# Kernel tuning notes

Hardware: AMD Instinct MI355X
Metric: run time of the kernel (lower is better)

## Reference

```python
import jax, jax.numpy as jnp
import numpy as np

DIM = 1024
KV_DIM = 768
NUM_HEADS = 16
HEAD_DIM = DIM // NUM_HEADS
EPS = 1e-6


def _rms_norm(h, g):
    var = jnp.mean(h * h, axis=-1, keepdims=True)
    return h * jax.lax.rsqrt(var + EPS) * g


def _rotate_half(t):
    t1, t2 = jnp.split(t, 2, axis=-1)
    return jnp.concatenate((-t2, t1), axis=-1)


def _apply_rope(t, cos, sin):
    # t: [B, L, H, D]; cos/sin: [B, L, D] -> broadcast over heads (unsqueeze_dim=2)
    cos = cos[:, :, None, :]
    sin = sin[:, :, None, :]
    return t * cos + _rotate_half(t) * sin


def setup_inputs() -> dict:
    key = jax.random.key(0)
    ks = jax.random.split(key, 16)
    B, Lq, Lkv = 2, 4096, 1024
    inp = {
        "x": jax.random.normal(ks[0], (B, Lq, DIM), jnp.float32),
        "y": jax.random.normal(ks[1], (B, Lkv, KV_DIM), jnp.float32),
        "x_cos": jax.random.normal(ks[2], (B, Lq, HEAD_DIM), jnp.float32),
        "x_sin": jax.random.normal(ks[3], (B, Lq, HEAD_DIM), jnp.float32),
        "y_cos": jax.random.normal(ks[4], (B, Lkv, HEAD_DIM), jnp.float32),
        "y_sin": jax.random.normal(ks[5], (B, Lkv, HEAD_DIM), jnp.float32),
        # Linear params stored as [in, out] (apply as h @ W + b)
        "Wq": jax.random.normal(ks[6], (DIM, DIM), jnp.float32) * 0.02,
        "bq": jnp.zeros((DIM,), jnp.float32),
        "Wk": jax.random.normal(ks[7], (KV_DIM, DIM), jnp.float32) * 0.02,
        "bk": jnp.zeros((DIM,), jnp.float32),
        "Wv": jax.random.normal(ks[8], (KV_DIM, DIM), jnp.float32) * 0.02,
        "bv": jnp.zeros((DIM,), jnp.float32),
        "Wo": jax.random.normal(ks[9], (DIM, DIM), jnp.float32) * 0.02,
        "bo": jnp.zeros((DIM,), jnp.float32),
        "gq": jnp.ones((DIM,), jnp.float32),   # RMSNorm weight for q
        "gk": jnp.ones((DIM,), jnp.float32),   # RMSNorm weight for k
    }
    return inp


def reference(x, y, x_cos, x_sin, y_cos, y_sin,
              Wq, bq, Wk, bk, Wv, bv, Wo, bo, gq, gk):
    B, Lq, _ = x.shape
    _, Lkv, _ = y.shape
    q = _rms_norm(x @ Wq + bq, gq)              # [B, Lq, DIM]
    k = _rms_norm(y @ Wk + bk, gk)              # [B, Lkv, DIM]
    v = y @ Wv + bv                              # [B, Lkv, DIM]

    q = q.reshape(B, Lq, NUM_HEADS, HEAD_DIM)
    k = k.reshape(B, Lkv, NUM_HEADS, HEAD_DIM)
    v = v.reshape(B, Lkv, NUM_HEADS, HEAD_DIM)

    q = _apply_rope(q, x_cos, x_sin)
    k = _apply_rope(k, y_cos, y_sin)

    scale = HEAD_DIM ** -0.5
    scores = jnp.einsum("blhd,bmhd->bhlm", q, k) * scale   # [B, H, Lq, Lkv]
    probs = jax.nn.softmax(scores, axis=-1)
    out = jnp.einsum("bhlm,bmhd->blhd", probs, v)           # [B, Lq, H, D]
    out = out.reshape(B, Lq, DIM)
    return out @ Wo + bo
```

## Files before the change

### kernel.cpp

```cpp
#include <hip/hip_runtime.h>

typedef __bf16 bf16;
typedef __bf16 bf16x4 __attribute__((ext_vector_type(4)));
typedef __bf16 bf16x8 __attribute__((ext_vector_type(8)));
typedef float  f32x4  __attribute__((ext_vector_type(4)));

#define NH   16
#define HD   64
#define DQ   1024
#define DKV  768
#define LQ   4096
#define LKV  1024
#define NB   2

__device__ __forceinline__ f32x4 mfma16(bf16x8 a, bf16x8 b, f32x4 c) {
    return __builtin_amdgcn_mfma_f32_16x16x32_bf16(a, b, c, 0, 0, 0);
}

#define GLDS16(g, l) __builtin_amdgcn_global_load_lds(                      \
    (const __attribute__((address_space(1))) void*)(g),                     \
    (__attribute__((address_space(3))) void*)(l), 16, 0, 0)

__global__ __launch_bounds__(256) void prep(
        const float* __restrict__ Wq, const float* __restrict__ Wk,
        const float* __restrict__ Wv, const float* __restrict__ Wo,
        bf16* __restrict__ Wq_t, bf16* __restrict__ Wk_t,
        bf16* __restrict__ Wv_t, bf16* __restrict__ Wo_t,
        const float* __restrict__ x, const float* __restrict__ y,
        bf16* __restrict__ xb, bf16* __restrict__ yb,
        int nx8, int ntot8) {
    if (blockIdx.z < 4) {
        __shared__ float tile[32][33];
        const float* in; bf16* out; int K;
        switch (blockIdx.z) {
            case 0:  in = Wq; out = Wq_t; K = DQ;  break;
            case 1:  in = Wk; out = Wk_t; K = DKV; break;
            case 2:  in = Wv; out = Wv_t; K = DKV; break;
            default: in = Wo; out = Wo_t; K = DQ;  break;
        }
        int n0 = blockIdx.x * 32, k0 = blockIdx.y * 32;
        if (k0 >= K) return;
        int tx = threadIdx.x, ty = threadIdx.y;
        for (int yy = 0; yy < 32; yy += 8)
            tile[ty + yy][tx] = in[(size_t)(k0 + ty + yy) * DQ + n0 + tx];
        __syncthreads();
        for (int yy = 0; yy < 32; yy += 8)
            out[(size_t)(n0 + ty + yy) * K + k0 + tx] = (bf16)tile[tx][ty + yy];
    } else {
        int tid = threadIdx.y * 32 + threadIdx.x;
        int flat = (blockIdx.y * 32 + blockIdx.x) * 256 + tid;
        for (int i = flat; i < ntot8; i += 32 * 32 * 256) {
            const float* in; bf16* out; int j;
            if (i < nx8) { in = x; out = xb; j = i; }
            else         { in = y; out = yb; j = i - nx8; }
            float4 a0 = ((const float4*)in)[(size_t)j * 2];
            float4 a1 = ((const float4*)in)[(size_t)j * 2 + 1];
            bf16x8 v = {(bf16)a0.x, (bf16)a0.y, (bf16)a0.z, (bf16)a0.w,
                        (bf16)a1.x, (bf16)a1.y, (bf16)a1.z, (bf16)a1.w};
            ((bf16x8*)out)[j] = v;
        }
    }
}

template <int MODE>
__device__ __forceinline__ void gemm_body(const bf16* __restrict__ A,
                                          const bf16* __restrict__ Bt,
                                          const float* __restrict__ bias,
                                          void* __restrict__ Cv,
                                          int N, int K, int m0) {
    __shared__ bf16 As[128 * 32];
    __shared__ bf16 Bs[128 * 32];
    int tid  = threadIdx.x;
    int lane = tid & 63, w = tid >> 6;
    int quad = lane >> 4, l15 = lane & 15;
    int wm = (w >> 1) * 64, wn = (w & 1) * 64;
    int n0 = blockIdx.x * 128;
    int srow = tid >> 2, scol = (tid & 3) * 8;
    const bf16* Ag = &A [(size_t)(m0 + srow) * K + scol];
    const bf16* Bg = &Bt[(size_t)(n0 + srow) * K + scol];
    bf16* Asw = As + w * 512;
    bf16* Bsw = Bs + w * 512;

    f32x4 acc[4][4] = {};

    for (int k0 = 0; k0 < K; k0 += 32) {
        GLDS16(Ag + k0,                  Asw);
        GLDS16(Ag + (size_t)64 * K + k0, Asw + 2048);
        GLDS16(Bg + k0,                  Bsw);
        GLDS16(Bg + (size_t)64 * K + k0, Bsw + 2048);
        __syncthreads();
        bf16x8 af[4], bfr[4];
#pragma unroll
        for (int i = 0; i < 4; i++)
            af[i] = *(const bf16x8*)&As[(size_t)(wm + i * 16 + l15) * 32 + quad * 8];
#pragma unroll
        for (int j = 0; j < 4; j++)
            bfr[j] = *(const bf16x8*)&Bs[(size_t)(wn + j * 16 + l15) * 32 + quad * 8];
#pragma unroll
        for (int i = 0; i < 4; i++)
#pragma unroll
            for (int j = 0; j < 4; j++)
                acc[i][j] = mfma16(af[i], bfr[j], acc[i][j]);
        __syncthreads();
    }

    bf16*  Cb = (bf16*)Cv;
    float* Cf = (float*)Cv;
#pragma unroll
    for (int i = 0; i < 4; i++)
#pragma unroll
        for (int j = 0; j < 4; j++) {
            int col = n0 + wn + j * 16 + l15;
            float bcol = bias[col];
            if (MODE == 1) {
                int rowb = m0 + wm + i * 16 + quad * 4;
                int bb = rowb >> 10, kv = rowb & 1023;
                int h = col >> 6, d = col & 63;
                bf16x4 val = {(bf16)(acc[i][j][0] + bcol), (bf16)(acc[i][j][1] + bcol),
                              (bf16)(acc[i][j][2] + bcol), (bf16)(acc[i][j][3] + bcol)};
                *(bf16x4*)&Cb[(((size_t)(bb * NH + h) * HD) + d) * LKV + kv] = val;
            } else {
#pragma unroll
                for (int r = 0; r < 4; r++) {
                    int row = m0 + wm + i * 16 + quad * 4 + r;
                    float v = acc[i][j][r] + bcol;
                    if (MODE == 2) Cf[(size_t)row * N + col] = v;
                    else           Cb[(size_t)row * N + col] = (bf16)v;
                }
            }
        }
}

__global__ __launch_bounds__(256) void gemm_qkv(
        const bf16* xb, const bf16* Wq_t, const float* bq, bf16* qbuf,
        const bf16* yb, const bf16* Wk_t, const float* bk, bf16* kbuf,
        const bf16* Wv_t, const float* bv, bf16* vT) {
    int y = blockIdx.y;
    if (y < 64)      gemm_body<0>(xb, Wq_t, bq, qbuf, DQ, DQ,  y * 128);
    else if (y < 80) gemm_body<0>(yb, Wk_t, bk, kbuf, DQ, DKV, (y - 64) * 128);
    else             gemm_body<1>(yb, Wv_t, bv, vT,   DQ, DKV, (y - 80) * 128);
}
__global__ __launch_bounds__(256) void gemm_o(const bf16* A, const bf16* Bt,
                                              const float* bias, void* Cv) {
    gemm_body<2>(A, Bt, bias, Cv, DQ, DQ, blockIdx.y * 128);
}

__global__ __launch_bounds__(256) void rmsnorm_rope3(bf16* __restrict__ qb,
                                                     bf16* __restrict__ kb,
                                                     const float* __restrict__ gq,
                                                     const float* __restrict__ gk,
                                                     const float* __restrict__ xc,
                                                     const float* __restrict__ xs,
                                                     const float* __restrict__ yc,
                                                     const float* __restrict__ ys) {
    int w = threadIdx.x >> 6, lane = threadIdx.x & 63;
    int row = blockIdx.x * 4 + w;
    bf16* t; const float *g, *cs, *sn;
    if (row < NB * LQ) {
        t = qb + (size_t)row * DQ; g = gq;
        cs = xc + (size_t)row * HD; sn = xs + (size_t)row * HD;
    } else {
        int r2 = row - NB * LQ;
        t = kb + (size_t)r2 * DQ; g = gk;
        cs = yc + (size_t)r2 * HD; sn = ys + (size_t)r2 * HD;
    }
    int c0 = lane * 16;
    bf16x8 a0 = *(const bf16x8*)&t[c0];
    bf16x8 a1 = *(const bf16x8*)&t[c0 + 8];
    float vv[16], ss = 0.f;
#pragma unroll
    for (int j = 0; j < 8; j++) { vv[j] = (float)a0[j]; vv[8 + j] = (float)a1[j]; }
#pragma unroll
    for (int j = 0; j < 16; j++) ss += vv[j] * vv[j];
#pragma unroll
    for (int off = 32; off >= 1; off >>= 1) ss += __shfl_xor(ss, off, 64);
    float rms = rsqrtf(ss * (1.0f / 1024.0f) + 1e-6f);
    float nv[16];
#pragma unroll
    for (int j = 0; j < 16; j++) nv[j] = vv[j] * rms * g[c0 + j];
    int d0 = (lane & 3) * 16;
    float sgn = (lane & 2) ? 1.f : -1.f;
    bf16x8 o0, o1;
#pragma unroll
    for (int j = 0; j < 16; j++) {
        float pv = __shfl_xor(nv[j], 2, 64);
        float r = nv[j] * cs[d0 + j] + sgn * pv * sn[d0 + j];
        if (j < 8) o0[j] = (bf16)r; else o1[j - 8] = (bf16)r;
    }
    *(bf16x8*)&t[c0]     = o0;
    *(bf16x8*)&t[c0 + 8] = o1;
}

__global__ __launch_bounds__(256) void attn_kern(const bf16* __restrict__ q,
                                                 const bf16* __restrict__ k,
                                                 const bf16* __restrict__ vT,
                                                 bf16* __restrict__ o) {
    __shared__ bf16 Ks[2][64][72];
    __shared__ bf16 Vs[2][64][72];
    __shared__ bf16 pbuf[4][2][16][72];
    int tid = threadIdx.x, w = tid >> 6, lane = tid & 63;
    int quad = lane >> 4, l15 = lane & 15;
    int b = blockIdx.z, h = blockIdx.y, qt = blockIdx.x;
    int qrow0 = qt * 128 + w * 16;

    bf16x8 qf[2][2];
#pragma unroll
    for (int tl = 0; tl < 2; tl++) {
        size_t qb = ((size_t)(b * LQ) + qrow0 + tl * 64 + l15) * DQ + h * HD;
        qf[tl][0] = *(const bf16x8*)&q[qb + quad * 8];
        qf[tl][1] = *(const bf16x8*)&q[qb + 32 + quad * 8];
#pragma unroll
        for (int e = 0; e < 8; e++) {
            qf[tl][0][e] = (bf16)((float)qf[tl][0][e] * 0.125f);
            qf[tl][1][e] = (bf16)((float)qf[tl][1][e] * 0.125f);
        }
    }

    int srow = tid >> 2, scol = (tid & 3) * 16;
    const bf16* kg = &k[((size_t)(b * LKV) + srow) * DQ + h * HD + scol];
    const bf16* vg = &vT[(((size_t)(b * NH + h) * HD) + srow) * LKV + scol];

    bf16x8 kr0 = *(const bf16x8*)kg;
    bf16x8 kr1 = *(const bf16x8*)(kg + 8);
    bf16x8 vr0 = *(const bf16x8*)vg;
    bf16x8 vr1 = *(const bf16x8*)(vg + 8);
    *(bf16x8*)&Ks[0][srow][scol]     = kr0;
    *(bf16x8*)&Ks[0][srow][scol + 8] = kr1;
    *(bf16x8*)&Vs[0][srow][scol]     = vr0;
    *(bf16x8*)&Vs[0][srow][scol + 8] = vr1;
    __syncthreads();

    f32x4 O[2][4] = {};
    float m_run[2] = {-1e30f, -1e30f}, l_run[2] = {0.f, 0.f};

    for (int i = 0; i < 16; i++) {
        int cur = i & 1;
        if (i < 15) {
            size_t ko = (size_t)(i + 1) * 64 * DQ;
            kr0 = *(const bf16x8*)(kg + ko);
            kr1 = *(const bf16x8*)(kg + ko + 8);
            vr0 = *(const bf16x8*)(vg + (i + 1) * 64);
            vr1 = *(const bf16x8*)(vg + (i + 1) * 64 + 8);
        }
        f32x4 S[2][4];
#pragma unroll
        for (int t = 0; t < 4; t++) {
            bf16x8 kf0 = *(const bf16x8*)&Ks[cur][t * 16 + l15][quad * 8];
            bf16x8 kf1 = *(const bf16x8*)&Ks[cur][t * 16 + l15][32 + quad * 8];
#pragma unroll
            for (int tl = 0; tl < 2; tl++) {
                f32x4 z = {};
                z = mfma16(kf0, qf[tl][0], z);
                S[tl][t] = mfma16(kf1, qf[tl][1], z);
            }
        }
#pragma unroll
        for (int tl = 0; tl < 2; tl++) {
            float mx = -1e30f;
#pragma unroll
            for (int t = 0; t < 4; t++)
#pragma unroll
                for (int r = 0; r < 4; r++) mx = fmaxf(mx, S[tl][t][r]);
            mx = fmaxf(mx, __shfl_xor(mx, 16, 64));
            mx = fmaxf(mx, __shfl_xor(mx, 32, 64));
            float mn = fmaxf(m_run[tl], mx);
            float alpha = __expf(m_run[tl] - mn);
            m_run[tl] = mn;
            float rs = 0.f;
#pragma unroll
            for (int t = 0; t < 4; t++) {
                float p0 = __expf(S[tl][t][0] - mn), p1 = __expf(S[tl][t][1] - mn);
                float p2 = __expf(S[tl][t][2] - mn), p3 = __expf(S[tl][t][3] - mn);
                rs += (p0 + p1) + (p2 + p3);
                bf16x4 pb4 = {(bf16)p0, (bf16)p1, (bf16)p2, (bf16)p3};
                *(bf16x4*)&pbuf[w][tl][l15][t * 16 + quad * 4] = pb4;
            }
            rs += __shfl_xor(rs, 16, 64);
            rs += __shfl_xor(rs, 32, 64);
            l_run[tl] = l_run[tl] * alpha + rs;
#pragma unroll
            for (int td = 0; td < 4; td++)
#pragma unroll
                for (int r = 0; r < 4; r++) O[tl][td][r] *= alpha;
        }
        asm volatile("s_waitcnt lgkmcnt(0)" ::: "memory");
#pragma unroll
        for (int tl = 0; tl < 2; tl++) {
            bf16x8 pf0 = *(const bf16x8*)&pbuf[w][tl][l15][quad * 8];
            bf16x8 pf1 = *(const bf16x8*)&pbuf[w][tl][l15][32 + quad * 8];
#pragma unroll
            for (int td = 0; td < 4; td++) {
                bf16x8 vf0 = *(const bf16x8*)&Vs[cur][td * 16 + l15][quad * 8];
                bf16x8 vf1 = *(const bf16x8*)&Vs[cur][td * 16 + l15][32 + quad * 8];
                O[tl][td] = mfma16(vf0, pf0, O[tl][td]);
                O[tl][td] = mfma16(vf1, pf1, O[tl][td]);
            }
        }
        if (i < 15) {
            int nxt = 1 - cur;
            *(bf16x8*)&Ks[nxt][srow][scol]     = kr0;
            *(bf16x8*)&Ks[nxt][srow][scol + 8] = kr1;
            *(bf16x8*)&Vs[nxt][srow][scol]     = vr0;
            *(bf16x8*)&Vs[nxt][srow][scol + 8] = vr1;
            __syncthreads();
        }
    }

#pragma unroll
    for (int tl = 0; tl < 2; tl++) {
        float inv = 1.0f / l_run[tl];
        size_t orow = ((size_t)(b * LQ) + qrow0 + tl * 64 + l15) * DQ + h * HD;
#pragma unroll
        for (int td = 0; td < 4; td++) {
            bf16x4 ov = {(bf16)(O[tl][td][0] * inv), (bf16)(O[tl][td][1] * inv),
                         (bf16)(O[tl][td][2] * inv), (bf16)(O[tl][td][3] * inv)};
            *(bf16x4*)&o[orow + td * 16 + quad * 4] = ov;
        }
    }
}

extern "C" void kernel_launch(void* const* d_in, const int* in_sizes, int n_in,
                              void* d_out, int out_size, void* d_ws, size_t ws_size,
                              hipStream_t stream) {
    const float* x     = (const float*)d_in[0];
    const float* y     = (const float*)d_in[1];
    const float* x_cos = (const float*)d_in[2];
    const float* x_sin = (const float*)d_in[3];
    const float* y_cos = (const float*)d_in[4];
    const float* y_sin = (const float*)d_in[5];
    const float* Wq    = (const float*)d_in[6];
    const float* bq    = (const float*)d_in[7];
    const float* Wk    = (const float*)d_in[8];
    const float* bk    = (const float*)d_in[9];
    const float* Wv    = (const float*)d_in[10];
    const float* bv    = (const float*)d_in[11];
    const float* Wo    = (const float*)d_in[12];
    const float* bo    = (const float*)d_in[13];
    const float* gq    = (const float*)d_in[14];
    const float* gk    = (const float*)d_in[15];

    char* ws = (char*)d_ws;
    bf16* Wq_t = (bf16*)ws;  ws += (size_t)DQ * DQ * 2;
    bf16* Wk_t = (bf16*)ws;  ws += (size_t)DQ * DKV * 2;
    bf16* Wv_t = (bf16*)ws;  ws += (size_t)DQ * DKV * 2;
    bf16* Wo_t = (bf16*)ws;  ws += (size_t)DQ * DQ * 2;
    bf16* qbuf = (bf16*)ws;  ws += (size_t)NB * LQ * DQ * 2;
    bf16* kbuf = (bf16*)ws;  ws += (size_t)NB * LKV * DQ * 2;
    bf16* vT   = (bf16*)ws;  ws += (size_t)NB * NH * HD * LKV * 2;
    bf16* aout = (bf16*)ws;  ws += (size_t)NB * LQ * DQ * 2;
    bf16* yb   = (bf16*)ws;  ws += (size_t)NB * LKV * DKV * 2;
    bf16* xb   = aout;

    int nx8 = NB * LQ * DQ / 8, ny8 = NB * LKV * DKV / 8;
    prep<<<dim3(32, 32, 5), dim3(32, 8), 0, stream>>>(
        Wq, Wk, Wv, Wo, Wq_t, Wk_t, Wv_t, Wo_t,
        x, y, xb, yb, nx8, nx8 + ny8);

    gemm_qkv<<<dim3(8, 96), 256, 0, stream>>>(
        xb, Wq_t, bq, qbuf, yb, Wk_t, bk, kbuf, Wv_t, bv, vT);

    rmsnorm_rope3<<<NB * (LQ + LKV) / 4, 256, 0, stream>>>(
        qbuf, kbuf, gq, gk, x_cos, x_sin, y_cos, y_sin);

    attn_kern<<<dim3(LQ / 128, NH, NB), 256, 0, stream>>>(qbuf, kbuf, vT, aout);

    gemm_o<<<dim3(DQ / 128, NB * LQ / 128), 256, 0, stream>>>(aout, Wo_t, bo, d_out);
}
```

Before: 299.3 us.

## Rewrite attention kernel with 32x32 MFMA, register-resident P, async LDS loads

The attention kernel switches from 16x16x32 to 32x32x16 bf16 MFMA, with each wave owning 32 query rows. The probability tile stays in registers: it is converted with packed bf16 conversion and rearranged with permlane32 swaps instead of a round trip through an LDS buffer. K and V tiles are loaded with global_load_lds into XOR-swizzled, unpadded shared memory, and softmax rescaling is skipped unless the running max grows by more than a threshold. Other changes include raising MFMA priority with s_setprio and requesting 4 blocks per CU through launch bounds. The aim is to cut LDS traffic and instruction overhead in the attention loop, at the cost of heavier register use and correctness that depends on the swizzle and lane-permute layout.

```diff
diff --git a/kernel.cpp b/kernel.cpp
--- a/kernel.cpp
+++ b/kernel.cpp
@@ -4,6 +4,8 @@
 typedef __bf16 bf16x4 __attribute__((ext_vector_type(4)));
 typedef __bf16 bf16x8 __attribute__((ext_vector_type(8)));
 typedef float  f32x4  __attribute__((ext_vector_type(4)));
+typedef float  f32x16 __attribute__((ext_vector_type(16)));
+typedef unsigned u32x4 __attribute__((ext_vector_type(4)));
 
 #define NH   16
 #define HD   64
@@ -15,6 +17,18 @@
 
 __device__ __forceinline__ f32x4 mfma16(bf16x8 a, bf16x8 b, f32x4 c) {
     return __builtin_amdgcn_mfma_f32_16x16x32_bf16(a, b, c, 0, 0, 0);
+}
+__device__ __forceinline__ f32x16 mfma32(bf16x8 a, bf16x8 b, f32x16 c) {
+    return __builtin_amdgcn_mfma_f32_32x32x16_bf16(a, b, c, 0, 0, 0);
+}
+
+__device__ __forceinline__ void plswap(unsigned &a, unsigned &b) {
+#if __has_builtin(__builtin_amdgcn_permlane32_swap)
+    auto r = __builtin_amdgcn_permlane32_swap(a, b, false, false);
+    a = (unsigned)r[0]; b = (unsigned)r[1];
+#else
+    asm volatile("v_permlane32_swap_b32 %0, %1" : "+v"(a), "+v"(b));
+#endif
 }
 
 #define GLDS16(g, l) __builtin_amdgcn_global_load_lds(                      \
@@ -191,130 +205,128 @@
     *(bf16x8*)&t[c0 + 8] = o1;
 }
 
-__global__ __launch_bounds__(256) void attn_kern(const bf16* __restrict__ q,
-                                                 const bf16* __restrict__ k,
-                                                 const bf16* __restrict__ vT,
-                                                 bf16* __restrict__ o) {
-    __shared__ bf16 Ks[2][64][72];
-    __shared__ bf16 Vs[2][64][72];
-    __shared__ bf16 pbuf[4][2][16][72];
+__global__ __launch_bounds__(256, 4) void attn_kern(const bf16* __restrict__ q,
+                                                    const bf16* __restrict__ k,
+                                                    const bf16* __restrict__ vT,
+                                                    bf16* __restrict__ o) {
+    __shared__ bf16 Ks[2][64][64];
+    __shared__ bf16 Vs[2][64][64];
     int tid = threadIdx.x, w = tid >> 6, lane = tid & 63;
-    int quad = lane >> 4, l15 = lane & 15;
+    int l31 = lane & 31, hi = lane >> 5;
     int b = blockIdx.z, h = blockIdx.y, qt = blockIdx.x;
-    int qrow0 = qt * 128 + w * 16;
-
-    bf16x8 qf[2][2];
-#pragma unroll
-    for (int tl = 0; tl < 2; tl++) {
-        size_t qb = ((size_t)(b * LQ) + qrow0 + tl * 64 + l15) * DQ + h * HD;
-        qf[tl][0] = *(const bf16x8*)&q[qb + quad * 8];
-        qf[tl][1] = *(const bf16x8*)&q[qb + 32 + quad * 8];
-#pragma unroll
-        for (int e = 0; e < 8; e++) {
-            qf[tl][0][e] = (bf16)((float)qf[tl][0][e] * 0.125f);
-            qf[tl][1][e] = (bf16)((float)qf[tl][1][e] * 0.125f);
-        }
-    }
-
-    int srow = tid >> 2, scol = (tid & 3) * 16;
-    const bf16* kg = &k[((size_t)(b * LKV) + srow) * DQ + h * HD + scol];
-    const bf16* vg = &vT[(((size_t)(b * NH + h) * HD) + srow) * LKV + scol];
-
-    bf16x8 kr0 = *(const bf16x8*)kg;
-    bf16x8 kr1 = *(const bf16x8*)(kg + 8);
-    bf16x8 vr0 = *(const bf16x8*)vg;
-    bf16x8 vr1 = *(const bf16x8*)(vg + 8);
-    *(bf16x8*)&Ks[0][srow][scol]     = kr0;
-    *(bf16x8*)&Ks[0][srow][scol + 8] = kr1;
-    *(bf16x8*)&Vs[0][srow][scol]     = vr0;
-    *(bf16x8*)&Vs[0][srow][scol + 8] = vr1;
+    int qrow = qt * 128 + w * 32 + l31;
+    int sw8 = (l31 & 7) << 3;
+
+    bf16x8 qf[4];
+    {
+        const bf16* qg = &q[((size_t)(b * LQ) + qrow) * DQ + h * HD + hi * 8];
+#pragma unroll
+        for (int kc = 0; kc < 4; kc++) {
+            bf16x8 tq = *(const bf16x8*)(qg + kc * 16);
+#pragma unroll
+            for (int e = 0; e < 8; e++) tq[e] = (bf16)((float)tq[e] * 0.125f);
+            qf[kc] = tq;
+        }
+    }
+
+    int rb = w * 16;
+    int srow = rb + (lane >> 3);
+    int sl = (lane & 7) ^ (srow & 7);
+    const bf16* kg0 = &k[((size_t)(b * LKV) + srow) * DQ + h * HD + sl * 8];
+    const bf16* vg0 = &vT[(((size_t)(b * NH + h) * HD) + srow) * LKV + sl * 8];
+
+    GLDS16(kg0,                   &Ks[0][rb][0]);
+    GLDS16(kg0 + (size_t)8 * DQ,  &Ks[0][rb + 8][0]);
+    GLDS16(vg0,                   &Vs[0][rb][0]);
+    GLDS16(vg0 + (size_t)8 * LKV, &Vs[0][rb + 8][0]);
     __syncthreads();
 
-    f32x4 O[2][4] = {};
-    float m_run[2] = {-1e30f, -1e30f}, l_run[2] = {0.f, 0.f};
+    f32x16 O0 = {}, O1 = {};
+    float m_run = -1e30f, l_run = 0.f;
 
     for (int i = 0; i < 16; i++) {
         int cur = i & 1;
         if (i < 15) {
+            int nxt = cur ^ 1;
             size_t ko = (size_t)(i + 1) * 64 * DQ;
-            kr0 = *(const bf16x8*)(kg + ko);
-            kr1 = *(const bf16x8*)(kg + ko + 8);
-            vr0 = *(const bf16x8*)(vg + (i + 1) * 64);
-            vr1 = *(const bf16x8*)(vg + (i + 1) * 64 + 8);
-        }
-        f32x4 S[2][4];
-#pragma unroll
-        for (int t = 0; t < 4; t++) {
-            bf16x8 kf0 = *(const bf16x8*)&Ks[cur][t * 16 + l15][quad * 8];
-            bf16x8 kf1 = *(const bf16x8*)&Ks[cur][t * 16 + l15][32 + quad * 8];
-#pragma unroll
-            for (int tl = 0; tl < 2; tl++) {
-                f32x4 z = {};
-                z = mfma16(kf0, qf[tl][0], z);
-                S[tl][t] = mfma16(kf1, qf[tl][1], z);
+            int    vo = (i + 1) * 64;
+            GLDS16(kg0 + ko,                   &Ks[nxt][rb][0]);
+            GLDS16(kg0 + ko + (size_t)8 * DQ,  &Ks[nxt][rb + 8][0]);
+            GLDS16(vg0 + vo,                   &Vs[nxt][rb][0]);
+            GLDS16(vg0 + vo + (size_t)8 * LKV, &Vs[nxt][rb + 8][0]);
+        }
+#pragma unroll
+        for (int t = 0; t < 2; t++) {
+            f32x16 S = {};
+            {
+                int krow = t * 32 + l31;
+                __builtin_amdgcn_s_setprio(1);
+#pragma unroll
+                for (int kc = 0; kc < 4; kc++) {
+                    bf16x8 kf = *(const bf16x8*)&Ks[cur][krow][(kc * 16 + hi * 8) ^ sw8];
+                    S = mfma32(kf, qf[kc], S);
+                }
+                __builtin_amdgcn_s_setprio(0);
             }
-        }
-#pragma unroll
-        for (int tl = 0; tl < 2; tl++) {
-            float mx = -1e30f;
-#pragma unroll
-            for (int t = 0; t < 4; t++)
-#pragma unroll
-                for (int r = 0; r < 4; r++) mx = fmaxf(mx, S[tl][t][r]);
-            mx = fmaxf(mx, __shfl_xor(mx, 16, 64));
-            mx = fmaxf(mx, __shfl_xor(mx, 32, 64));
-            float mn = fmaxf(m_run[tl], mx);
-            float alpha = __expf(m_run[tl] - mn);
-            m_run[tl] = mn;
+            float m01 = fmaxf(fmaxf(S[0], S[1]),  fmaxf(S[2], S[3]));
+            float m23 = fmaxf(fmaxf(S[4], S[5]),  fmaxf(S[6], S[7]));
+            float m45 = fmaxf(fmaxf(S[8], S[9]),  fmaxf(S[10], S[11]));
+            float m67 = fmaxf(fmaxf(S[12], S[13]), fmaxf(S[14], S[15]));
+            float pmax = fmaxf(fmaxf(m01, m23), fmaxf(m45, m67));
+            pmax = fmaxf(pmax, __shfl_xor(pmax, 32, 64));
+            if (!__all(pmax - m_run <= 8.f)) {
+                float mn = fmaxf(m_run, pmax);
+                float alpha = __expf(m_run - mn);
+                m_run = mn; l_run *= alpha;
+#pragma unroll
+                for (int r = 0; r < 16; r++) { O0[r] *= alpha; O1[r] *= alpha; }
+            }
             float rs = 0.f;
 #pragma unroll
-            for (int t = 0; t < 4; t++) {
-                float p0 = __expf(S[tl][t][0] - mn), p1 = __expf(S[tl][t][1] - mn);
-                float p2 = __expf(S[tl][t][2] - mn), p3 = __expf(S[tl][t][3] - mn);
-                rs += (p0 + p1) + (p2 + p3);
-                bf16x4 pb4 = {(bf16)p0, (bf16)p1, (bf16)p2, (bf16)p3};
-                *(bf16x4*)&pbuf[w][tl][l15][t * 16 + quad * 4] = pb4;
+            for (int r = 0; r < 16; r++) { S[r] = __expf(S[r] - m_run); rs += S[r]; }
+            rs += __shfl_xor(rs, 32, 64);
+            l_run += rs;
+            unsigned dw[8];
+#pragma unroll
+            for (int g = 0; g < 4; g++)
+#pragma unroll
+                for (int hh = 0; hh < 2; hh++) {
+                    unsigned d_;
+                    asm("v_cvt_pk_bf16_f32 %0, %1, %2"
+                        : "=v"(d_) : "v"(S[4 * g + 2 * hh]), "v"(S[4 * g + 2 * hh + 1]));
+                    dw[g * 2 + hh] = d_;
+                }
+#pragma unroll
+            for (int kcl = 0; kcl < 2; kcl++) {
+                int kc = t * 2 + kcl;
+                unsigned a0 = dw[(2 * kcl) * 2 + 0], b0 = dw[(2 * kcl + 1) * 2 + 0];
+                unsigned a1 = dw[(2 * kcl) * 2 + 1], b1 = dw[(2 * kcl + 1) * 2 + 1];
+                plswap(a0, b0);
+                plswap(a1, b1);
+                u32x4 pw = {a0, a1, b0, b1};
+                bf16x8 pb = __builtin_bit_cast(bf16x8, pw);
+                int vcol = (kc * 16 + hi * 8) ^ sw8;
+                bf16x8 vf0 = *(const bf16x8*)&Vs[cur][l31][vcol];
+                bf16x8 vf1 = *(const bf16x8*)&Vs[cur][32 + l31][vcol];
+                __builtin_amdgcn_s_setprio(1);
+                O0 = mfma32(vf0, pb, O0);
+                O1 = mfma32(vf1, pb, O1);
+                __builtin_amdgcn_s_setprio(0);
             }
-            rs += __shfl_xor(rs, 16, 64);
-            rs += __shfl_xor(rs, 32, 64);
-            l_run[tl] = l_run[tl] * alpha + rs;
-#pragma unroll
-            for (int td = 0; td < 4; td++)
-#pragma unroll
-                for (int r = 0; r < 4; r++) O[tl][td][r] *= alpha;
-        }
-        asm volatile("s_waitcnt lgkmcnt(0)" ::: "memory");
-#pragma unroll
-        for (int tl = 0; tl < 2; tl++) {
-            bf16x8 pf0 = *(const bf16x8*)&pbuf[w][tl][l15][quad * 8];
-            bf16x8 pf1 = *(const bf16x8*)&pbuf[w][tl][l15][32 + quad * 8];
-#pragma unroll
-            for (int td = 0; td < 4; td++) {
-                bf16x8 vf0 = *(const bf16x8*)&Vs[cur][td * 16 + l15][quad * 8];
-                bf16x8 vf1 = *(const bf16x8*)&Vs[cur][td * 16 + l15][32 + quad * 8];
-                O[tl][td] = mfma16(vf0, pf0, O[tl][td]);
-                O[tl][td] = mfma16(vf1, pf1, O[tl][td]);
-            }
-        }
-        if (i < 15) {
-            int nxt = 1 - cur;
-            *(bf16x8*)&Ks[nxt][srow][scol]     = kr0;
-            *(bf16x8*)&Ks[nxt][srow][scol + 8] = kr1;
-            *(bf16x8*)&Vs[nxt][srow][scol]     = vr0;
-            *(bf16x8*)&Vs[nxt][srow][scol + 8] = vr1;
-            __syncthreads();
-        }
-    }
-
-#pragma unroll
-    for (int tl = 0; tl < 2; tl++) {
-        float inv = 1.0f / l_run[tl];
-        size_t orow = ((size_t)(b * LQ) + qrow0 + tl * 64 + l15) * DQ + h * HD;
-#pragma unroll
-        for (int td = 0; td < 4; td++) {
-            bf16x4 ov = {(bf16)(O[tl][td][0] * inv), (bf16)(O[tl][td][1] * inv),
-                         (bf16)(O[tl][td][2] * inv), (bf16)(O[tl][td][3] * inv)};
-            *(bf16x4*)&o[orow + td * 16 + quad * 4] = ov;
+        }
+        if (i < 15) __syncthreads();
+    }
+
+    float inv = 1.0f / l_run;
+    size_t ob = ((size_t)(b * LQ) + qrow) * DQ + h * HD;
+#pragma unroll
+    for (int td = 0; td < 2; td++) {
+        const f32x16& O = td ? O1 : O0;
+#pragma unroll
+        for (int g = 0; g < 4; g++) {
+            bf16x4 ov = {(bf16)(O[4 * g + 0] * inv), (bf16)(O[4 * g + 1] * inv),
+                         (bf16)(O[4 * g + 2] * inv), (bf16)(O[4 * g + 3] * inv)};
+            *(bf16x4*)&o[ob + td * 32 + g * 8 + hi * 4] = ov;
         }
     }
 }
```

After: 282.9 us. 1.06x faster.
